# Kernel optimization log

Measured on AMD Instinct MI355X. Metric: run time of the kernel, lower is better.

## Reference

```python
import jax, jax.numpy as jnp
import numpy as np

B, NQ, T, D, H, L = 2, 4, 1024, 1024, 16, 8
CARD, N_COND, COND_D, WIN = 1024, 64, 768, 5
DFF = 4 * D


def _ln(x, g, b):
    m = jnp.mean(x, axis=-1, keepdims=True)
    v = jnp.var(x, axis=-1, keepdims=True)
    return (x - m) * jax.lax.rsqrt(v + 1e-5) * g + b


def _mha(qx, kx, vx, Wq, bq, Wk, bk, Wv, bv, Wo, bo, mask):
    # qx:(B,Tq,D) kx/vx:(B,Tk,*)
    Bq, Tq = qx.shape[0], qx.shape[1]
    Tk = kx.shape[1]
    hd = D // H
    q = (qx @ Wq + bq).reshape(Bq, Tq, H, hd)
    k = (kx @ Wk + bk).reshape(Bq, Tk, H, hd)
    v = (vx @ Wv + bv).reshape(Bq, Tk, H, hd)
    s = jnp.einsum('bthd,bshd->bhts', q, k) / jnp.sqrt(jnp.float32(hd))
    if mask is not None:
        s = s + mask  # additive banded mask (0 in-band, -inf outside)
    p = jax.nn.softmax(s, axis=-1)
    o = jnp.einsum('bhts,bshd->bthd', p, v).reshape(Bq, Tq, D)
    return o @ Wo + bo


def _pos_emb(t, d):
    # matches get_sinusoidal_positional_embeddings: interleaved sin/cos
    i = jnp.arange(d // 2, dtype=jnp.float32) * 2.0
    p = jnp.arange(t, dtype=jnp.float32)[:, None]
    theta = p / (10000.0 ** (i / d))[None, :]  # (t, d/2)
    return jnp.stack([jnp.sin(theta), jnp.cos(theta)], axis=-1).reshape(t, d)[None]


def _band_mask(t, w):
    # magnet_restricted_att_mask with shift=0: log(tril(triu(1, -w), w))
    idx = jnp.arange(t)
    dlt = idx[None, :] - idx[:, None]
    return jnp.where((dlt >= -w) & (dlt <= w), 0.0, -jnp.inf).astype(jnp.float32)


def _forward(x, cond, emb,
             ln1_g, ln1_b, sWq, sbq, sWk, sbk, sWv, sbv, sWo, sbo,
             ln2_g, ln2_b, cWq, cbq, cWk, cbk, cWv, cbv, cWo, cbo,
             ln3_g, ln3_b, W1, b1, W2, b2, out_g, out_b, headW, headb):
    # multi-codebook embedding sum: (B,NQ,T) -> (B,T,D)
    h = emb[0][x[:, 0]]
    for q in range(1, NQ):
        h = h + emb[q][x[:, q]]
    h = h + _pos_emb(T, D).astype(h.dtype)
    mask = _band_mask(T, WIN)
    for l in range(L):
        sin = _ln(h, ln1_g[l], ln1_b[l])
        h = h + _mha(sin, sin, sin, sWq[l], sbq[l], sWk[l], sbk[l],
                     sWv[l], sbv[l], sWo[l], sbo[l], mask)
        cin = _ln(h, ln2_g[l], ln2_b[l])
        h = h + _mha(cin, cond, cond, cWq[l], cbq[l], cWk[l], cbk[l],
                     cWv[l], cbv[l], cWo[l], cbo[l], None)
        fin = _ln(h, ln3_g[l], ln3_b[l])
        h = h + (jax.nn.gelu(fin @ W1[l] + b1[l], approximate=True) @ W2[l] + b2[l])
    h = _ln(h, out_g, out_b)
    # per-codebook heads -> (B, NQ, T, CARD)
    return jnp.einsum('btd,qdk->bqtk', h, headW) + headb[None, :, None, :]


def setup_inputs() -> dict:
    key = jax.random.key(0)
    ks = iter(jax.random.split(key, 40))
    s = 0.02
    nrm = lambda shape: jax.random.normal(next(ks), shape, dtype=jnp.float32) * s
    inp = {}
    inp['x'] = jax.random.randint(next(ks), (B, NQ, T), 0, CARD + 1)
    inp['cond'] = jax.random.normal(next(ks), (B, N_COND, COND_D), dtype=jnp.float32)
    inp['emb'] = nrm((NQ, CARD + 1, D))
    for nm in ('ln1', 'ln2', 'ln3'):
        inp[nm + '_g'] = jnp.ones((L, D), jnp.float32)
        inp[nm + '_b'] = jnp.zeros((L, D), jnp.float32)
    # self-attn projections
    inp['sWq'], inp['sWk'], inp['sWv'], inp['sWo'] = (nrm((L, D, D)) for _ in range(4))
    inp['sbq'] = jnp.zeros((L, D), jnp.float32); inp['sbk'] = jnp.zeros((L, D), jnp.float32)
    inp['sbv'] = jnp.zeros((L, D), jnp.float32); inp['sbo'] = jnp.zeros((L, D), jnp.float32)
    # cross-attn projections (k/v act on cond_dim)
    inp['cWq'] = nrm((L, D, D)); inp['cWk'] = nrm((L, COND_D, D))
    inp['cWv'] = nrm((L, COND_D, D)); inp['cWo'] = nrm((L, D, D))
    inp['cbq'] = jnp.zeros((L, D), jnp.float32); inp['cbk'] = jnp.zeros((L, D), jnp.float32)
    inp['cbv'] = jnp.zeros((L, D), jnp.float32); inp['cbo'] = jnp.zeros((L, D), jnp.float32)
    inp['W1'] = nrm((L, D, DFF)); inp['b1'] = jnp.zeros((L, DFF), jnp.float32)
    inp['W2'] = nrm((L, DFF, D)); inp['b2'] = jnp.zeros((L, D), jnp.float32)
    inp['out_g'] = jnp.ones((D,), jnp.float32); inp['out_b'] = jnp.zeros((D,), jnp.float32)
    inp['headW'] = nrm((NQ, D, CARD)); inp['headb'] = jnp.zeros((NQ, CARD), jnp.float32)
    return inp


def reference(x, cond, emb,
              ln1_g, ln1_b, sWq, sbq, sWk, sbk, sWv, sbv, sWo, sbo,
              ln2_g, ln2_b, cWq, cbq, cWk, cbk, cWv, cbv, cWo, cbo,
              ln3_g, ln3_b, W1, b1, W2, b2, out_g, out_b, headW, headb):
    return _forward(x, cond, emb,
                    ln1_g, ln1_b, sWq, sbq, sWk, sbk, sWv, sbv, sWo, sbo,
                    ln2_g, ln2_b, cWq, cbq, cWk, cbk, cWv, cbv, cWo, cbo,
                    ln3_g, ln3_b, W1, b1, W2, b2, out_g, out_b, headW, headb)
```

## Files before the change

### kernel.cpp

```cpp
#include <hip/hip_runtime.h>
#include <math.h>

#define BATCH   2
#define NQ_CB   4
#define T_SEQ   1024
#define DMODEL  1024
#define NHEAD   16
#define HDIM    64
#define NLAYER  8
#define CARD_SZ 1024
#define NCOND   64
#define CONDD   768
#define DFF_SZ  4096
#define WIN     5

typedef __attribute__((ext_vector_type(8))) short bf16x8;
typedef __attribute__((ext_vector_type(4))) float f32x4;
typedef unsigned short ushortx;

__device__ inline short f2bf(float f) {
  union { float f; unsigned u; } c;
  c.f = f;
  unsigned r = (c.u + 0x7FFFu + ((c.u >> 16) & 1u)) >> 16;
  return (short)r;
}
__device__ inline float bf2f(unsigned short u) {
  union { unsigned u; float f; } c;
  c.u = ((unsigned)u) << 16;
  return c.f;
}

__device__ inline void gld_lds16(const void* g, void* s) {
  __builtin_amdgcn_global_load_lds(
      (const __attribute__((address_space(1))) void*)g,
      (__attribute__((address_space(3))) void*)s, 16, 0, 0);
}

template <int N> __device__ inline void s_wait_vmcnt() {
  asm volatile("s_waitcnt vmcnt(%0)" :: "n"(N) : "memory");
}

__device__ inline void blk_bar() {
  asm volatile("" ::: "memory");
  __builtin_amdgcn_s_barrier();
  asm volatile("" ::: "memory");
}

__global__ __launch_bounds__(256) void pack_kernel(
    const float* __restrict__ src, short* __restrict__ dst, int K, int N)
{
  size_t matoff = (size_t)blockIdx.z * K * N;
  src += matoff; dst += matoff;
  int gid = blockIdx.x * 256 + threadIdx.x;
  int slab = gid >> 6, cell = gid & 63;
  int KT = K >> 5;
  int ng = slab / KT, kt = slab - ng * KT;
  int n = ng * 16 + (cell & 15);
  int k = kt * 32 + (cell >> 4) * 8;
  bf16x8 pk;
#pragma unroll
  for (int j = 0; j < 8; ++j) pk[j] = f2bf(src[(size_t)(k + j) * N + n]);
  *(bf16x8*)&dst[(size_t)gid * 8] = pk;
}

__global__ __launch_bounds__(256) void embed_kernel(
    const int* __restrict__ x, const float* __restrict__ emb,
    float* __restrict__ h)
{
  int bt = blockIdx.x;
  int b = bt >> 10, t = bt & (T_SEQ - 1);
  int tid = threadIdx.x;
  float4 acc = make_float4(0.f, 0.f, 0.f, 0.f);
#pragma unroll
  for (int q = 0; q < NQ_CB; ++q) {
    int idx = x[(b * NQ_CB + q) * T_SEQ + t];
    const float4* er =
        (const float4*)(emb + ((size_t)q * (CARD_SZ + 1) + idx) * DMODEL);
    float4 e = er[tid];
    acc.x += e.x; acc.y += e.y; acc.z += e.z; acc.w += e.w;
  }
  int d0 = tid * 4;
  float c = -logf(10000.f) * (2.f / (float)DMODEL);
  float th0 = (float)t * expf(c * (float)(d0 >> 1));
  float th1 = (float)t * expf(c * (float)((d0 + 2) >> 1));
  acc.x += sinf(th0); acc.y += cosf(th0);
  acc.z += sinf(th1); acc.w += cosf(th1);
  ((float4*)(h + (size_t)bt * DMODEL))[tid] = acc;
}

__global__ __launch_bounds__(256) void ln_kernel(
    const float* __restrict__ x, const float* __restrict__ g,
    const float* __restrict__ b, ushortx* __restrict__ y)
{
  int row = blockIdx.x;
  int tid = threadIdx.x;
  const float4* xr = (const float4*)(x + (size_t)row * DMODEL);
  float4 v = xr[tid];
  float s  = v.x + v.y + v.z + v.w;
  float ss = v.x * v.x + v.y * v.y + v.z * v.z + v.w * v.w;
#pragma unroll
  for (int off = 32; off; off >>= 1) {
    s  += __shfl_xor(s, off, 64);
    ss += __shfl_xor(ss, off, 64);
  }
  __shared__ float sh_s[4], sh_ss[4];
  int w = tid >> 6;
  if ((tid & 63) == 0) { sh_s[w] = s; sh_ss[w] = ss; }
  __syncthreads();
  s  = sh_s[0] + sh_s[1] + sh_s[2] + sh_s[3];
  ss = sh_ss[0] + sh_ss[1] + sh_ss[2] + sh_ss[3];
  float mean = s * (1.f / DMODEL);
  float var  = ss * (1.f / DMODEL) - mean * mean;
  float rstd = rsqrtf(var + 1e-5f);
  float4 gv = ((const float4*)g)[tid];
  float4 bv = ((const float4*)b)[tid];
  ushort4 o;
  o.x = (ushortx)f2bf((v.x - mean) * rstd * gv.x + bv.x);
  o.y = (ushortx)f2bf((v.y - mean) * rstd * gv.y + bv.y);
  o.z = (ushortx)f2bf((v.z - mean) * rstd * gv.z + bv.z);
  o.w = (ushortx)f2bf((v.w - mean) * rstd * gv.w + bv.w);
  *(ushort4*)(y + (size_t)row * DMODEL + tid * 4) = o;
}

#define FL_GELU  1
#define FL_REMAP 2
#define FL_OBF16 4

template <int MW, int ABF16>
__global__ __launch_bounds__(256, 2) void gemm_pk(
    const void* __restrict__ Ain,
    const short* __restrict__ Wp0, const short* __restrict__ Wp1,
    const short* __restrict__ Wp2, long wstride, int nw,
    const float* __restrict__ b0, const float* __restrict__ b1,
    const float* __restrict__ b2, long bstride,
    const float* __restrict__ resid,
    void* __restrict__ C0v, void* __restrict__ C1v, void* __restrict__ C2v,
    long cstride,
    int M, int N, int K, int flags)
{
  __shared__ __align__(16) short Als[2][MW * 2048];
  __shared__ __align__(16) short Bls[2][8192];

  int tid = threadIdx.x;
  int z = blockIdx.z;
  int w = z % nw, li = z / nw;
  const short* Wp = (w == 0 ? Wp0 : (w == 1 ? Wp1 : Wp2)) + (size_t)li * wstride;
  const float* bias = (w == 0 ? b0 : (w == 1 ? b1 : b2)) + (size_t)li * bstride;
  char* Cb = (char*)(w == 0 ? C0v : (w == 1 ? C1v : C2v)) + (size_t)li * cstride;

  int bm = blockIdx.y * (MW * 32);
  int bn = blockIdx.x * 128;
  int wave = tid >> 6, lane = tid & 63;
  int wm = (wave >> 1) * (MW * 16);
  int wn = (wave & 1) * 64;
  int KT = K >> 5;
  const int NT = K >> 6;
  constexpr int NSTG = 4 + (ABF16 ? MW : 0);

  f32x4 acc[MW][4];
#pragma unroll
  for (int i = 0; i < MW; ++i)
#pragma unroll
    for (int j = 0; j < 4; ++j) {
      acc[i][j][0] = 0.f; acc[i][j][1] = 0.f;
      acc[i][j][2] = 0.f; acc[i][j][3] = 0.f;
    }

  auto stage = [&](int kt, int buf) {
#pragma unroll
    for (int i = 0; i < 4; ++i) {
      int s = wave * 4 + i;
      const short* src =
          Wp + ((size_t)((bn >> 4) + (s >> 1)) * KT + 2 * kt + (s & 1)) * 512 +
          lane * 8;
      gld_lds16(src, &Bls[buf][s * 512]);
    }
    if (ABF16) {
      const ushortx* A16 = (const ushortx*)Ain;
#pragma unroll
      for (int i = 0; i < MW; ++i) {
        int s = wave * MW + i;
        const ushortx* src = A16 +
            (size_t)(bm + (s >> 1) * 16 + (lane & 15)) * K +
            kt * 64 + (s & 1) * 32 + (lane >> 4) * 8;
        gld_lds16(src, &Als[buf][s * 512]);
      }
    } else {
      const float* Af = (const float*)Ain;
      int m = tid >> 2, kq = tid & 3;
#pragma unroll
      for (int ks = 0; ks < 2; ++ks) {
        const float* src = Af + (size_t)(bm + m) * K + kt * 64 + ks * 32 + kq * 8;
        float4 f0 = *(const float4*)src;
        float4 f1 = *(const float4*)(src + 4);
        bf16x8 pk;
        pk[0] = f2bf(f0.x); pk[1] = f2bf(f0.y); pk[2] = f2bf(f0.z); pk[3] = f2bf(f0.w);
        pk[4] = f2bf(f1.x); pk[5] = f2bf(f1.y); pk[6] = f2bf(f1.z); pk[7] = f2bf(f1.w);
        *(bf16x8*)&Als[buf][((m >> 4) * 2 + ks) * 512 + ((m & 15) | (kq << 4)) * 8] = pk;
      }
    }
  };

  stage(0, 0);
  int cur = 0;

  for (int kt = 0; kt < NT; ++kt) {
    if (kt + 1 < NT) {
      stage(kt + 1, cur ^ 1);
      if (ABF16) s_wait_vmcnt<NSTG>();
      else       s_wait_vmcnt<0>();
    } else {
      s_wait_vmcnt<0>();
    }
    if (!ABF16) asm volatile("s_waitcnt lgkmcnt(0)" ::: "memory");
    blk_bar();

#pragma unroll
    for (int ks = 0; ks < 2; ++ks) {
      bf16x8 af[MW], bfr[4];
#pragma unroll
      for (int i = 0; i < MW; ++i)
        af[i] = *(bf16x8*)&Als[cur][(((wm >> 4) + i) * 2 + ks) * 512 + lane * 8];
#pragma unroll
      for (int j = 0; j < 4; ++j)
        bfr[j] = *(bf16x8*)&Bls[cur][(((wn >> 4) + j) * 2 + ks) * 512 + lane * 8];
#pragma unroll
      for (int i = 0; i < MW; ++i)
#pragma unroll
        for (int j = 0; j < 4; ++j)
          acc[i][j] = __builtin_amdgcn_mfma_f32_16x16x32_bf16(
              af[i], bfr[j], acc[i][j], 0, 0, 0);
    }
    blk_bar();
    cur ^= 1;
  }

  int quad = lane >> 4, col = lane & 15;
#pragma unroll
  for (int i = 0; i < MW; ++i) {
    int m0 = bm + wm + i * 16 + quad * 4;
#pragma unroll
    for (int j = 0; j < 4; ++j) {
      int n0 = bn + wn + j * 16 + col;
      float bval = bias[n0];
#pragma unroll
      for (int r = 0; r < 4; ++r) {
        int m = m0 + r;
        float v = acc[i][j][r] + bval;
        if (flags & FL_GELU) {
          v = 0.5f * v *
              (1.f + tanhf(0.7978845608028654f * (v + 0.044715f * v * v * v)));
        }
        if (resid) v += resid[(size_t)m * N + n0];
        size_t row;
        if (flags & FL_REMAP)
          row = ((size_t)(m >> 10) * NQ_CB + li) * T_SEQ + (m & (T_SEQ - 1));
        else
          row = m;
        if (flags & FL_OBF16)
          ((ushortx*)Cb)[row * N + n0] = (ushortx)f2bf(v);
        else
          ((float*)Cb)[row * N + n0] = v;
      }
    }
  }
}

__global__ __launch_bounds__(256) void self_attn_kernel(
    const ushortx* __restrict__ q, const ushortx* __restrict__ k,
    const ushortx* __restrict__ v, ushortx* __restrict__ o)
{
  int w = blockIdx.x * 4 + (threadIdx.x >> 6);
  int lane = threadIdx.x & 63;
  int t = w & (T_SEQ - 1);
  int bh = w >> 10;
  int h = bh & (NHEAD - 1);
  int b = bh >> 4;
  size_t base = ((size_t)(b * T_SEQ) * DMODEL) + h * HDIM + lane;
  float qv = bf2f(q[base + (size_t)t * DMODEL]);

  float sc[2 * WIN + 1];
  float mx = -1e30f;
#pragma unroll
  for (int j = 0; j < 2 * WIN + 1; ++j) {
    int s = t - WIN + j;
    float d;
    if (s >= 0 && s < T_SEQ) {
      float kv = bf2f(k[base + (size_t)s * DMODEL]);
      d = qv * kv;
#pragma unroll
      for (int off = 32; off; off >>= 1) d += __shfl_xor(d, off, 64);
      d *= 0.125f;
    } else {
      d = -1e30f;
    }
    sc[j] = d;
    mx = fmaxf(mx, d);
  }
  float sum = 0.f;
#pragma unroll
  for (int j = 0; j < 2 * WIN + 1; ++j) {
    sc[j] = expf(sc[j] - mx);
    sum += sc[j];
  }
  float inv = 1.f / sum;
  float ov = 0.f;
#pragma unroll
  for (int j = 0; j < 2 * WIN + 1; ++j) {
    int s = t - WIN + j;
    if (s >= 0 && s < T_SEQ) ov += sc[j] * bf2f(v[base + (size_t)s * DMODEL]);
  }
  o[base + (size_t)t * DMODEL] = (ushortx)f2bf(ov * inv);
}

__global__ __launch_bounds__(256) void cross_attn_kernel(
    const ushortx* __restrict__ q, const ushortx* __restrict__ k,
    const ushortx* __restrict__ v, ushortx* __restrict__ o)
{
  int w = blockIdx.x * 4 + (threadIdx.x >> 6);
  int lane = threadIdx.x & 63;
  int t = w & (T_SEQ - 1);
  int h = (w >> 10) & (NHEAD - 1);
  int b = w >> 14;
  size_t qoff = ((size_t)(b * T_SEQ + t) * DMODEL) + h * HDIM;
  float qv = bf2f(q[qoff + lane]);

  const ushortx* krow = k + ((size_t)(b * NCOND + lane) * DMODEL) + h * HDIM;
  float s_l = 0.f;
#pragma unroll
  for (int d = 0; d < HDIM; ++d) {
    float qd = __shfl(qv, d, 64);
    s_l += qd * bf2f(krow[d]);
  }
  s_l *= 0.125f;
  float m = s_l;
#pragma unroll
  for (int off = 32; off; off >>= 1) m = fmaxf(m, __shfl_xor(m, off, 64));
  float p = expf(s_l - m);
  float sum = p;
#pragma unroll
  for (int off = 32; off; off >>= 1) sum += __shfl_xor(sum, off, 64);
  p /= sum;

  float ov = 0.f;
  const ushortx* vb = v + ((size_t)(b * NCOND) * DMODEL) + h * HDIM + lane;
#pragma unroll
  for (int s = 0; s < NCOND; ++s) {
    float ps = __shfl(p, s, 64);
    ov += ps * bf2f(vb[(size_t)s * DMODEL]);
  }
  o[qoff + lane] = (ushortx)f2bf(ov);
}

static void gemm_launch(hipStream_t st, int MW, int abf16,
    const void* A, const short* W0, const short* W1, const short* W2,
    long wstride, int nw,
    const float* b0, const float* b1, const float* b2, long bstride,
    const float* resid, void* C0, void* C1, void* C2, long cstride,
    int M, int N, int K, int z, int flags)
{
  dim3 grid(N / 128, M / (MW * 32), z);
  if (MW == 4)
    hipLaunchKernelGGL((gemm_pk<4, 1>), grid, dim3(256), 0, st, A, W0, W1, W2,
                       wstride, nw, b0, b1, b2, bstride, resid, C0, C1, C2,
                       cstride, M, N, K, flags);
  else if (abf16)
    hipLaunchKernelGGL((gemm_pk<2, 1>), grid, dim3(256), 0, st, A, W0, W1, W2,
                       wstride, nw, b0, b1, b2, bstride, resid, C0, C1, C2,
                       cstride, M, N, K, flags);
  else
    hipLaunchKernelGGL((gemm_pk<2, 0>), grid, dim3(256), 0, st, A, W0, W1, W2,
                       wstride, nw, b0, b1, b2, bstride, resid, C0, C1, C2,
                       cstride, M, N, K, flags);
}

extern "C" void kernel_launch(void* const* d_in, const int* in_sizes, int n_in,
                              void* d_out, int out_size, void* d_ws, size_t ws_size,
                              hipStream_t stream)
{
  const int*   x     = (const int*)  d_in[0];
  const float* cond  = (const float*)d_in[1];
  const float* emb   = (const float*)d_in[2];
  const float* ln1_g = (const float*)d_in[3];
  const float* ln1_b = (const float*)d_in[4];
  const float* ln2_g = (const float*)d_in[5];
  const float* ln2_b = (const float*)d_in[6];
  const float* ln3_g = (const float*)d_in[7];
  const float* ln3_b = (const float*)d_in[8];
  const float* sWq   = (const float*)d_in[9];
  const float* sWk   = (const float*)d_in[10];
  const float* sWv   = (const float*)d_in[11];
  const float* sWo   = (const float*)d_in[12];
  const float* sbq   = (const float*)d_in[13];
  const float* sbk   = (const float*)d_in[14];
  const float* sbv   = (const float*)d_in[15];
  const float* sbo   = (const float*)d_in[16];
  const float* cWq   = (const float*)d_in[17];
  const float* cWk   = (const float*)d_in[18];
  const float* cWv   = (const float*)d_in[19];
  const float* cWo   = (const float*)d_in[20];
  const float* cbq   = (const float*)d_in[21];
  const float* cbk   = (const float*)d_in[22];
  const float* cbv   = (const float*)d_in[23];
  const float* cbo   = (const float*)d_in[24];
  const float* W1    = (const float*)d_in[25];
  const float* b1    = (const float*)d_in[26];
  const float* W2    = (const float*)d_in[27];
  const float* b2    = (const float*)d_in[28];
  const float* out_g = (const float*)d_in[29];
  const float* out_b = (const float*)d_in[30];
  const float* headW = (const float*)d_in[31];
  const float* headb = (const float*)d_in[32];

  float* out = (float*)d_out;
  const size_t MB = 1u << 20;
  const long MAT = 1048576L;
  const long CMAT = 768L * 1024;
  const long FMAT = 4L * 1048576;
  const int M = BATCH * T_SEQ;

  char* wsb = (char*)d_ws;
  float*   h   = (float*)(wsb);
  ushortx* tmp = (ushortx*)(wsb + 8 * MB);
  ushortx* qb  = (ushortx*)(wsb + 12 * MB);
  ushortx* kb  = (ushortx*)(wsb + 16 * MB);
  ushortx* vb  = (ushortx*)(wsb + 20 * MB);
  ushortx* ao  = (ushortx*)(wsb + 24 * MB);
  ushortx* ffn = qb;
  ushortx* ckv = (ushortx*)(wsb + 28 * MB);
  short*   PB  = (short*)(wsb + 32 * MB);

  bool big = ws_size >= (size_t)32 * MB + (size_t)268435456;

  auto pack = [&](const float* src, short* dst, int K, int N, int z) {
    hipLaunchKernelGGL(pack_kernel, dim3((unsigned)((size_t)K * N / 2048), 1, z),
                       dim3(256), 0, stream, src, dst, K, N);
  };

  short *Pq = PB, *Pk = PB + 8 * MAT, *Pv = PB + 16 * MAT, *Po = PB + 24 * MAT;
  short *Pcq = PB + 32 * MAT, *Pco = PB + 40 * MAT;
  short *Pck = PB + 48 * MAT, *Pcv = PB + 54 * MAT;
  short *Pw1 = PB + 60 * MAT, *Pw2 = PB + 92 * MAT, *Phd = PB + 124 * MAT;
  if (big) {
    pack(sWq, Pq, 1024, 1024, 8);  pack(sWk, Pk, 1024, 1024, 8);
    pack(sWv, Pv, 1024, 1024, 8);  pack(sWo, Po, 1024, 1024, 8);
    pack(cWq, Pcq, 1024, 1024, 8); pack(cWo, Pco, 1024, 1024, 8);
    pack(cWk, Pck, 768, 1024, 8);  pack(cWv, Pcv, 768, 1024, 8);
    pack(W1, Pw1, 1024, 4096, 8);  pack(W2, Pw2, 4096, 1024, 8);
    pack(headW, Phd, 1024, 1024, 4);
  }

  hipLaunchKernelGGL(embed_kernel, dim3(M), dim3(256), 0, stream, x, emb, h);

  if (big) {
    gemm_launch(stream, 2, 0, cond, Pck, Pcv, nullptr, CMAT, 2,
                cbk, cbv, nullptr, 1024, nullptr,
                ckv, (char*)ckv + 262144, nullptr, 524288,
                BATCH * NCOND, DMODEL, CONDD, 16, FL_OBF16);
  } else {
    pack(cWk, PB, 768, 1024, 8);
    gemm_launch(stream, 2, 0, cond, PB, nullptr, nullptr, CMAT, 1,
                cbk, nullptr, nullptr, 1024, nullptr,
                ckv, nullptr, nullptr, 524288,
                BATCH * NCOND, DMODEL, CONDD, 8, FL_OBF16);
    pack(cWv, PB, 768, 1024, 8);
    gemm_launch(stream, 2, 0, cond, PB, nullptr, nullptr, CMAT, 1,
                cbv, nullptr, nullptr, 1024, nullptr,
                (char*)ckv + 262144, nullptr, nullptr, 524288,
                BATCH * NCOND, DMODEL, CONDD, 8, FL_OBF16);
  }

  const int attn_blocks = BATCH * NHEAD * T_SEQ / 4;

  for (int l = 0; l < NLAYER; ++l) {
    const float* L1g = ln1_g + l * DMODEL, *L1b = ln1_b + l * DMODEL;
    const float* L2g = ln2_g + l * DMODEL, *L2b = ln2_b + l * DMODEL;
    const float* L3g = ln3_g + l * DMODEL, *L3b = ln3_b + l * DMODEL;

    hipLaunchKernelGGL(ln_kernel, dim3(M), dim3(256), 0, stream, h, L1g, L1b, tmp);
    {
      const short *wq, *wk, *wv;
      if (big) { wq = Pq + l * MAT; wk = Pk + l * MAT; wv = Pv + l * MAT; }
      else {
        pack(sWq + (size_t)l * MAT, PB, 1024, 1024, 1);
        pack(sWk + (size_t)l * MAT, PB + MAT, 1024, 1024, 1);
        pack(sWv + (size_t)l * MAT, PB + 2 * MAT, 1024, 1024, 1);
        wq = PB; wk = PB + MAT; wv = PB + 2 * MAT;
      }
      gemm_launch(stream, 4, 1, tmp, wq, wk, wv, 0, 3,
                  sbq + l * DMODEL, sbk + l * DMODEL, sbv + l * DMODEL, 0,
                  nullptr, qb, kb, vb, 0, M, DMODEL, DMODEL, 3, FL_OBF16);
    }
    hipLaunchKernelGGL(self_attn_kernel, dim3(attn_blocks), dim3(256), 0, stream,
                       qb, kb, vb, ao);
    {
      const short* wo = big ? Po + l * MAT : PB;
      if (!big) pack(sWo + (size_t)l * MAT, PB, 1024, 1024, 1);
      gemm_launch(stream, 2, 1, ao, wo, nullptr, nullptr, 0, 1,
                  sbo + l * DMODEL, nullptr, nullptr, 0,
                  h, h, nullptr, nullptr, 0, M, DMODEL, DMODEL, 1, 0);
    }

    hipLaunchKernelGGL(ln_kernel, dim3(M), dim3(256), 0, stream, h, L2g, L2b, tmp);
    {
      const short* wcq = big ? Pcq + l * MAT : PB;
      if (!big) pack(cWq + (size_t)l * MAT, PB, 1024, 1024, 1);
      gemm_launch(stream, 2, 1, tmp, wcq, nullptr, nullptr, 0, 1,
                  cbq + l * DMODEL, nullptr, nullptr, 0,
                  nullptr, qb, nullptr, nullptr, 0, M, DMODEL, DMODEL, 1, FL_OBF16);
    }
    hipLaunchKernelGGL(cross_attn_kernel, dim3(attn_blocks), dim3(256), 0, stream,
                       qb, ckv + (size_t)(2 * l) * 131072,
                       ckv + (size_t)(2 * l + 1) * 131072, ao);
    {
      const short* wco = big ? Pco + l * MAT : PB;
      if (!big) pack(cWo + (size_t)l * MAT, PB, 1024, 1024, 1);
      gemm_launch(stream, 2, 1, ao, wco, nullptr, nullptr, 0, 1,
                  cbo + l * DMODEL, nullptr, nullptr, 0,
                  h, h, nullptr, nullptr, 0, M, DMODEL, DMODEL, 1, 0);
    }

    hipLaunchKernelGGL(ln_kernel, dim3(M), dim3(256), 0, stream, h, L3g, L3b, tmp);
    {
      const short* w1p = big ? Pw1 + l * FMAT : PB;
      if (!big) pack(W1 + (size_t)l * FMAT, PB, 1024, 4096, 1);
      gemm_launch(stream, 4, 1, tmp, w1p, nullptr, nullptr, 0, 1,
                  b1 + l * DFF_SZ, nullptr, nullptr, 0,
                  nullptr, ffn, nullptr, nullptr, 0,
                  M, DFF_SZ, DMODEL, 1, FL_GELU | FL_OBF16);
      const short* w2p = big ? Pw2 + l * FMAT : PB;
      if (!big) pack(W2 + (size_t)l * FMAT, PB, 4096, 1024, 1);
      gemm_launch(stream, 2, 1, ffn, w2p, nullptr, nullptr, 0, 1,
                  b2 + l * DMODEL, nullptr, nullptr, 0,
                  h, h, nullptr, nullptr, 0, M, DMODEL, DFF_SZ, 1, 0);
    }
  }

  hipLaunchKernelGGL(ln_kernel, dim3(M), dim3(256), 0, stream, h, out_g, out_b, tmp);
  {
    const short* whd = big ? Phd : PB;
    if (!big) pack(headW, PB, 1024, 1024, 4);
    gemm_launch(stream, 4, 1, tmp, whd, nullptr, nullptr, MAT, 1,
                headb, nullptr, nullptr, CARD_SZ, nullptr,
                out, nullptr, nullptr, 0, M, CARD_SZ, DMODEL, 4, FL_REMAP);
  }
}
```

Measured before the change: 3.373 ms.

## Add 4-stage LDS pipeline for bf16 GEMM and XCD-aware block remap

Makes the GEMM's LDS buffer depth a template parameter and adds a multi-stage prefetch loop with one barrier per k-step. The MW=2 bf16 path now uses four buffers, so more global loads are in flight to hide memory latency. Separately, block IDs are remapped so consecutive blocks land on the same XCD (the 8-way interleave) and share tiles in cache. The deeper pipeline uses more shared memory, which may cut occupancy below the two blocks per CU in the launch bounds. The remap assumes the block count is divisible by 8.

```diff
diff --git a/kernel.cpp b/kernel.cpp
--- a/kernel.cpp
+++ b/kernel.cpp
@@ -126,7 +126,7 @@
 #define FL_REMAP 2
 #define FL_OBF16 4
 
-template <int MW, int ABF16>
+template <int MW, int ABF16, int DEPTH>
 __global__ __launch_bounds__(256, 2) void gemm_pk(
     const void* __restrict__ Ain,
     const short* __restrict__ Wp0, const short* __restrict__ Wp1,
@@ -138,8 +138,8 @@
     long cstride,
     int M, int N, int K, int flags)
 {
-  __shared__ __align__(16) short Als[2][MW * 2048];
-  __shared__ __align__(16) short Bls[2][8192];
+  __shared__ __align__(16) short Als[DEPTH][MW * 2048];
+  __shared__ __align__(16) short Bls[DEPTH][8192];
 
   int tid = threadIdx.x;
   int z = blockIdx.z;
@@ -148,8 +148,16 @@
   const float* bias = (w == 0 ? b0 : (w == 1 ? b1 : b2)) + (size_t)li * bstride;
   char* Cb = (char*)(w == 0 ? C0v : (w == 1 ? C1v : C2v)) + (size_t)li * cstride;
 
-  int bm = blockIdx.y * (MW * 32);
-  int bn = blockIdx.x * 128;
+  int gx = gridDim.x, gy = gridDim.y;
+  int id = blockIdx.y * gx + blockIdx.x;
+  int nwg = gx * gy;
+  int qc = nwg >> 3;
+  int lin = (id & 7) * qc + (id >> 3);
+  int bxi = lin / gy;
+  int byi = lin - bxi * gy;
+
+  int bm = byi * (MW * 32);
+  int bn = bxi * 128;
   int wave = tid >> 6, lane = tid & 63;
   int wm = (wave >> 1) * (MW * 16);
   int wn = (wave & 1) * 64;
@@ -201,29 +209,16 @@
     }
   };
 
-  stage(0, 0);
-  int cur = 0;
-
-  for (int kt = 0; kt < NT; ++kt) {
-    if (kt + 1 < NT) {
-      stage(kt + 1, cur ^ 1);
-      if (ABF16) s_wait_vmcnt<NSTG>();
-      else       s_wait_vmcnt<0>();
-    } else {
-      s_wait_vmcnt<0>();
-    }
-    if (!ABF16) asm volatile("s_waitcnt lgkmcnt(0)" ::: "memory");
-    blk_bar();
-
+  auto compute = [&](int buf) {
 #pragma unroll
     for (int ks = 0; ks < 2; ++ks) {
       bf16x8 af[MW], bfr[4];
 #pragma unroll
       for (int i = 0; i < MW; ++i)
-        af[i] = *(bf16x8*)&Als[cur][(((wm >> 4) + i) * 2 + ks) * 512 + lane * 8];
+        af[i] = *(bf16x8*)&Als[buf][(((wm >> 4) + i) * 2 + ks) * 512 + lane * 8];
 #pragma unroll
       for (int j = 0; j < 4; ++j)
-        bfr[j] = *(bf16x8*)&Bls[cur][(((wn >> 4) + j) * 2 + ks) * 512 + lane * 8];
+        bfr[j] = *(bf16x8*)&Bls[buf][(((wn >> 4) + j) * 2 + ks) * 512 + lane * 8];
 #pragma unroll
       for (int i = 0; i < MW; ++i)
 #pragma unroll
@@ -231,8 +226,37 @@
           acc[i][j] = __builtin_amdgcn_mfma_f32_16x16x32_bf16(
               af[i], bfr[j], acc[i][j], 0, 0, 0);
     }
-    blk_bar();
-    cur ^= 1;
+  };
+
+  if constexpr (DEPTH == 2) {
+    stage(0, 0);
+    int cur = 0;
+    for (int kt = 0; kt < NT; ++kt) {
+      if (kt + 1 < NT) {
+        stage(kt + 1, cur ^ 1);
+        if (ABF16) s_wait_vmcnt<NSTG>();
+        else       s_wait_vmcnt<0>();
+      } else {
+        s_wait_vmcnt<0>();
+      }
+      if (!ABF16) asm volatile("s_waitcnt lgkmcnt(0)" ::: "memory");
+      blk_bar();
+      compute(cur);
+      blk_bar();
+      cur ^= 1;
+    }
+  } else {
+#pragma unroll
+    for (int p = 0; p < DEPTH - 1; ++p)
+      if (p < NT) stage(p, p);
+    for (int kt = 0; kt < NT; ++kt) {
+      if (kt + (DEPTH - 2) < NT) s_wait_vmcnt<(DEPTH - 2) * NSTG>();
+      else                       s_wait_vmcnt<0>();
+      blk_bar();
+      if (kt + DEPTH - 1 < NT)
+        stage(kt + DEPTH - 1, (kt + DEPTH - 1) & (DEPTH - 1));
+      compute(kt & (DEPTH - 1));
+    }
   }
 
   int quad = lane >> 4, col = lane & 15;
@@ -361,15 +385,15 @@
 {
   dim3 grid(N / 128, M / (MW * 32), z);
   if (MW == 4)
-    hipLaunchKernelGGL((gemm_pk<4, 1>), grid, dim3(256), 0, st, A, W0, W1, W2,
+    hipLaunchKernelGGL((gemm_pk<4, 1, 2>), grid, dim3(256), 0, st, A, W0, W1, W2,
                        wstride, nw, b0, b1, b2, bstride, resid, C0, C1, C2,
                        cstride, M, N, K, flags);
   else if (abf16)
-    hipLaunchKernelGGL((gemm_pk<2, 1>), grid, dim3(256), 0, st, A, W0, W1, W2,
+    hipLaunchKernelGGL((gemm_pk<2, 1, 4>), grid, dim3(256), 0, st, A, W0, W1, W2,
                        wstride, nw, b0, b1, b2, bstride, resid, C0, C1, C2,
                        cstride, M, N, K, flags);
   else
-    hipLaunchKernelGGL((gemm_pk<2, 0>), grid, dim3(256), 0, st, A, W0, W1, W2,
+    hipLaunchKernelGGL((gemm_pk<2, 0, 2>), grid, dim3(256), 0, st, A, W0, W1, W2,
                        wstride, nw, b0, b1, b2, bstride, resid, C0, C1, C2,
                        cstride, M, N, K, flags);
 }
```

New measurement: 3.400 ms. No clear change (+0.8%).
